# Kernel tuning notes

Hardware: AMD Instinct MI355X
Metric: run time of the kernel (lower is better)

The kernel has to match this reference:

```python
import jax, jax.numpy as jnp
import numpy as np
from functools import partial

L, D, H, F, K, T = 8, 512, 8, 2048, 11, 2048
DK = D // H
PAD = (K - 1) // 2  # 5, matches pad_zeros width
SCALE = DK ** -0.5  # q,k each prescaled by d_k^-0.25 in the torch code


def setup_inputs() -> dict:
    key = jax.random.key(0)
    ks = jax.random.split(key, 16)
    s = 0.02
    return {
        "x": jax.random.normal(ks[0], (1, T, D), jnp.float32),
        "ln1_g": jnp.ones((L, D), jnp.float32),
        "ln1_b": jnp.zeros((L, D), jnp.float32),
        "Wqkv": jax.random.normal(ks[1], (L, D, 3 * D), jnp.float32) * s,
        "bqkv": jnp.zeros((L, 3 * D), jnp.float32),
        "fsmn_w": jax.random.normal(ks[2], (L, D, K), jnp.float32) * s,
        "Wout": jax.random.normal(ks[3], (L, D, D), jnp.float32) * s,
        "bout": jnp.zeros((L, D), jnp.float32),
        "ln2_g": jnp.ones((L, D), jnp.float32),
        "ln2_b": jnp.zeros((L, D), jnp.float32),
        "W1": jax.random.normal(ks[4], (L, D, F), jnp.float32) * s,
        "b1": jnp.zeros((L, F), jnp.float32),
        "W2": jax.random.normal(ks[5], (L, F, D), jnp.float32) * s,
        "b2": jnp.zeros((L, D), jnp.float32),
        "after_g": jnp.ones((D,), jnp.float32),
        "after_b": jnp.zeros((D,), jnp.float32),
    }


def layernorm(x, g, b, eps=1e-5):
    m = jnp.mean(x, axis=-1, keepdims=True)
    v = jnp.var(x, axis=-1, keepdims=True)
    return (x - m) * jax.lax.rsqrt(v + eps) * g + b


def fsmn(v, w):
    # v: [1, T, D]; depthwise conv1d, kernel K, zero-pad PAD each side (matches pad_zeros cat)
    vc = jnp.transpose(v, (0, 2, 1))  # [1, D, T]
    out = jax.lax.conv_general_dilated(
        vc, w[:, None, :], window_strides=(1,), padding=[(PAD, PAD)],
        feature_group_count=D, dimension_numbers=("NCH", "OIH", "NCH"))
    return jnp.transpose(out, (0, 2, 1)) + v  # fsmn_block(...) + v


def encoder_layer(x, p):
    (g1, b1_, Wqkv, bqkv, fw, Wout, bout, g2, b2_, W1, c1, W2, c2) = p
    x1 = layernorm(x, g1, b1_)
    qkv = jnp.einsum("btd,de->bte", x1, Wqkv) + bqkv  # [1, T, 3D]
    q, k, v = jnp.split(qkv, 3, axis=-1)
    qh = q.reshape(T, H, DK).transpose(1, 0, 2)  # [H, T, dk]
    kh = k.reshape(T, H, DK).transpose(1, 0, 2)
    vh = v.reshape(T, H, DK).transpose(1, 0, 2)
    scores = jnp.einsum("htd,hsd->hts", qh, kh) * SCALE  # [H, T, T]
    attn = jnp.einsum("hts,hsd->htd", jax.nn.softmax(scores, axis=-1), vh)
    attn = attn.transpose(1, 0, 2).reshape(1, T, D)
    attn = jnp.einsum("btd,de->bte", attn, Wout) + bout
    mem = fsmn(v, fw)
    x = x + attn + mem
    h = layernorm(x, g2, b2_)
    h = jax.nn.relu(jnp.einsum("btd,df->btf", h, W1) + c1)
    x = x + jnp.einsum("btf,fd->btd", h, W2) + c2
    return x, None


def reference(x, ln1_g, ln1_b, Wqkv, bqkv, fsmn_w, Wout, bout, ln2_g, ln2_b, W1, b1, W2, b2, after_g, after_b):
    params = (ln1_g, ln1_b, Wqkv, bqkv, fsmn_w, Wout, bout, ln2_g, ln2_b, W1, b1, W2, b2)
    x, _ = jax.lax.scan(encoder_layer, x, params)
    return layernorm(x, after_g, after_b)
```

## Files before the change

kernel.cpp:

```cpp
#include <hip/hip_runtime.h>

using u16 = unsigned short;
using u32 = unsigned int;

typedef __bf16 bf16x8 __attribute__((ext_vector_type(8)));
typedef float f32x4 __attribute__((ext_vector_type(4)));

typedef __attribute__((address_space(3))) u32 as3_u32;
typedef __attribute__((address_space(1))) const u32 as1_u32;

__device__ __forceinline__ u16 f2bf(float f) {
  u32 u = __builtin_bit_cast(u32, f);
  u = u + 0x7FFFu + ((u >> 16) & 1u);
  return (u16)(u >> 16);
}
__device__ __forceinline__ float bf2f(u16 h) {
  return __builtin_bit_cast(float, (u32)h << 16);
}

__device__ __forceinline__ void gload16(const u16* g, u16* l) {
  __builtin_amdgcn_global_load_lds((as1_u32*)g, (as3_u32*)l, 16, 0, 0);
}

__global__ __launch_bounds__(256) void transpose_f32_bf16(
    const float* __restrict__ in, u16* __restrict__ out, int R, int C) {
  __shared__ u16 tile[32][33];
  long zofs = (long)blockIdx.z * R * C;
  int c0 = blockIdx.x * 32, r0 = blockIdx.y * 32;
  for (int i = threadIdx.y; i < 32; i += 8)
    tile[i][threadIdx.x] = f2bf(in[zofs + (long)(r0 + i) * C + c0 + threadIdx.x]);
  __syncthreads();
  for (int i = threadIdx.y; i < 32; i += 8)
    out[zofs + (long)(c0 + i) * R + r0 + threadIdx.x] = tile[threadIdx.x][i];
}

template <int MI, int NI, int VT>
__global__ __launch_bounds__(256) void gemm_bt(
    const u16* __restrict__ A, int lda,
    const u16* __restrict__ B, int ldb,
    const float* __restrict__ bias,
    u16* __restrict__ outBf, int ldob,
    float* __restrict__ outF, int ldof, int accF,
    u16* __restrict__ vtOut,
    int M, int N, int K, int kChunks, float scale, int relu) {
  __shared__ u16 As[MI * 32 * 64];
  __shared__ u16 Bs[NI * 32 * 64];
  __shared__ u16 Ts[VT ? NI * 32 : 1][72];
  const int m0 = blockIdx.y * (MI * 32), n0 = blockIdx.x * (NI * 32);
  const int tid = threadIdx.x, lane = tid & 63, wid = tid >> 6;
  const int wr = (wid >> 1) * (MI * 16), wc = (wid & 1) * (NI * 16);
  const int r16 = lane & 15, kg = lane >> 4;

  const int lrow = lane >> 3;
  const int lchunk = (lane & 7) ^ lrow;

  f32x4 acc[MI][NI];
#pragma unroll
  for (int i = 0; i < MI; ++i)
#pragma unroll
    for (int j = 0; j < NI; ++j) acc[i][j] = f32x4{0.f, 0.f, 0.f, 0.f};

  const int kcs = K / kChunks;
  const int kbase = kcs * blockIdx.z;
  const int nkt = kcs / 64;
  for (int kt = 0; kt < nkt; ++kt) {
    const int k0 = kbase + kt * 64;
    __syncthreads();
#pragma unroll
    for (int i = 0; i < MI; ++i) {
      const int r = i * 32 + wid * 8 + lrow;
      gload16(A + (long)(m0 + r) * lda + k0 + lchunk * 8, &As[wid * 512 + i * 2048]);
    }
#pragma unroll
    for (int j = 0; j < NI; ++j) {
      const int r = j * 32 + wid * 8 + lrow;
      gload16(B + (long)(n0 + r) * ldb + k0 + lchunk * 8, &Bs[wid * 512 + j * 2048]);
    }
    __syncthreads();

#pragma unroll
    for (int s = 0; s < 2; ++s) {
      bf16x8 af[MI], bfv[NI];
#pragma unroll
      for (int i = 0; i < MI; ++i) {
        const int r = wr + i * 16 + r16;
        af[i] = *reinterpret_cast<const bf16x8*>(
            &As[r * 64 + (((s * 4 + kg) ^ (r & 7)) << 3)]);
      }
#pragma unroll
      for (int j = 0; j < NI; ++j) {
        const int r = wc + j * 16 + r16;
        bfv[j] = *reinterpret_cast<const bf16x8*>(
            &Bs[r * 64 + (((s * 4 + kg) ^ (r & 7)) << 3)]);
      }
      __builtin_amdgcn_s_setprio(1);
#pragma unroll
      for (int i = 0; i < MI; ++i)
#pragma unroll
        for (int j = 0; j < NI; ++j)
          acc[i][j] = __builtin_amdgcn_mfma_f32_16x16x32_bf16(af[i], bfv[j], acc[i][j], 0, 0, 0);
      __builtin_amdgcn_s_setprio(0);
    }
  }

  const int rg = (lane >> 4) * 4;
  const bool doVT = VT && (n0 >= 1024);
#pragma unroll
  for (int i = 0; i < MI; ++i) {
#pragma unroll
    for (int j = 0; j < NI; ++j) {
      int col = n0 + wc + j * 16 + r16;
      float bv = (bias && blockIdx.z == 0) ? bias[col] : 0.f;
#pragma unroll
      for (int r = 0; r < 4; ++r) {
        int row = m0 + wr + i * 16 + rg + r;
        float v = acc[i][j][r] * scale + bv;
        if (outF) {
          long idx = (long)row * ldof + col;
          if (accF) atomicAdd(&outF[idx], v);
          else outF[idx] = v;
        }
        if (outBf) {
          if (relu && v < 0.f) v = 0.f;
          u16 hv = f2bf(v);
          outBf[(long)row * ldob + col] = hv;
          if (doVT) Ts[wc + j * 16 + r16][wr + i * 16 + rg + r] = hv;
        }
      }
    }
  }

  if constexpr (VT) {
    if (doVT) {
      __syncthreads();
      const int d0 = n0 - 1024;
      constexpr int CH = MI * 4;
      constexpr int TOT = NI * 32 * CH;
#pragma unroll
      for (int c = 0; c < TOT / 256; ++c) {
        int idx = tid * (TOT / 256) + c;
        int drow = idx / CH, off = (idx % CH) * 8;
        *reinterpret_cast<uint4*>(vtOut + (long)(d0 + drow) * 2048 + m0 + off) =
            *reinterpret_cast<const uint4*>(&Ts[drow][off]);
      }
    }
  }
}

constexpr int AFP = 72;

__global__ __launch_bounds__(256, 4) void flash_attn_split(
    const u16* __restrict__ qkv, const u16* __restrict__ vT,
    float* __restrict__ oPart, float* __restrict__ lPart) {
  __shared__ u16 Ks[2][64 * AFP];
  __shared__ u16 Vs[64 * AFP];
  __shared__ u16 Ps[4][16 * AFP];
  const int h = blockIdx.y;
  const int q0 = blockIdx.x * 64;
  const int split = blockIdx.z;
  const int tid = threadIdx.x;
  const int lane = tid & 63, wid = tid >> 6;
  const int r16 = lane & 15, kg8 = (lane >> 4) * 8;

  bf16x8 qa0, qa1;
  {
    union U { uint4 v; u16 hh[8]; } a, b;
    const u16* qrow = qkv + (long)(q0 + wid * 16 + r16) * 1536 + 64 * h;
    a.v = *reinterpret_cast<const uint4*>(qrow + kg8);
    b.v = *reinterpret_cast<const uint4*>(qrow + 32 + kg8);
#pragma unroll
    for (int i = 0; i < 8; ++i) {
      a.hh[i] = f2bf(bf2f(a.hh[i]) * 0.125f);
      b.hh[i] = f2bf(bf2f(b.hh[i]) * 0.125f);
    }
    qa0 = __builtin_bit_cast(bf16x8, a.v);
    qa1 = __builtin_bit_cast(bf16x8, b.v);
  }

  const int srow = tid >> 2;
  const int scol = (tid & 3) * 16;
  const u16* kgl = qkv + 512 + 64 * h + scol;
  const u16* vgl = vT + (long)(64 * h + srow) * 2048 + scol;

  uint4 kr0, kr1, vr0, vr1;
  auto LOAD = [&](int g) {
    const u16* kp = kgl + (long)(g * 64 + srow) * 1536;
    kr0 = *reinterpret_cast<const uint4*>(kp);
    kr1 = *reinterpret_cast<const uint4*>(kp + 8);
    const u16* vp = vgl + g * 64;
    vr0 = *reinterpret_cast<const uint4*>(vp);
    vr1 = *reinterpret_cast<const uint4*>(vp + 8);
  };
  auto STOREK = [&](int b) {
    *reinterpret_cast<uint4*>(&Ks[b][srow * AFP + scol]) = kr0;
    *reinterpret_cast<uint4*>(&Ks[b][srow * AFP + scol + 8]) = kr1;
  };
  auto STOREV = [&]() {
    *reinterpret_cast<uint4*>(&Vs[srow * AFP + scol]) = vr0;
    *reinterpret_cast<uint4*>(&Vs[srow * AFP + scol + 8]) = vr1;
  };

  f32x4 oacc[4];
#pragma unroll
  for (int j = 0; j < 4; ++j) oacc[j] = f32x4{0.f, 0.f, 0.f, 0.f};
  float lsum[4] = {0.f, 0.f, 0.f, 0.f};

  const int g0 = split * 8;
  LOAD(g0);
  STOREK(0);
  STOREV();
  __syncthreads();

  for (int t = 0; t < 8; ++t) {
    const int cur = t & 1;
    if (t < 7) LOAD(g0 + t + 1);

    f32x4 sacc[4];
#pragma unroll
    for (int j = 0; j < 4; ++j) sacc[j] = f32x4{0.f, 0.f, 0.f, 0.f};
    __builtin_amdgcn_s_setprio(1);
#pragma unroll
    for (int j = 0; j < 4; ++j) {
      bf16x8 b0 = *reinterpret_cast<const bf16x8*>(&Ks[cur][(j * 16 + r16) * AFP + kg8]);
      bf16x8 b1 = *reinterpret_cast<const bf16x8*>(&Ks[cur][(j * 16 + r16) * AFP + 32 + kg8]);
      sacc[j] = __builtin_amdgcn_mfma_f32_16x16x32_bf16(qa0, b0, sacc[j], 0, 0, 0);
      sacc[j] = __builtin_amdgcn_mfma_f32_16x16x32_bf16(qa1, b1, sacc[j], 0, 0, 0);
    }
    __builtin_amdgcn_s_setprio(0);

#pragma unroll
    for (int r = 0; r < 4; ++r) {
      float e0 = __expf(sacc[0][r]);
      float e1 = __expf(sacc[1][r]);
      float e2 = __expf(sacc[2][r]);
      float e3 = __expf(sacc[3][r]);
      lsum[r] += (e0 + e1) + (e2 + e3);
      int prow = (lane >> 4) * 4 + r;
      Ps[wid][prow * AFP + r16] = f2bf(e0);
      Ps[wid][prow * AFP + 16 + r16] = f2bf(e1);
      Ps[wid][prow * AFP + 32 + r16] = f2bf(e2);
      Ps[wid][prow * AFP + 48 + r16] = f2bf(e3);
    }

#pragma unroll
    for (int st = 0; st < 2; ++st) {
      bf16x8 pa = *reinterpret_cast<const bf16x8*>(&Ps[wid][r16 * AFP + st * 32 + kg8]);
      __builtin_amdgcn_s_setprio(1);
#pragma unroll
      for (int j = 0; j < 4; ++j) {
        bf16x8 bv = *reinterpret_cast<const bf16x8*>(&Vs[(j * 16 + r16) * AFP + st * 32 + kg8]);
        oacc[j] = __builtin_amdgcn_mfma_f32_16x16x32_bf16(pa, bv, oacc[j], 0, 0, 0);
      }
      __builtin_amdgcn_s_setprio(0);
    }

    if (t < 7) {
      STOREK(cur ^ 1);
      __syncthreads();
      STOREV();
      __syncthreads();
    }
  }

  const int rg = (lane >> 4) * 4;
#pragma unroll
  for (int r = 0; r < 4; ++r) {
    float ls = lsum[r];
#pragma unroll
    for (int o = 1; o < 16; o <<= 1) ls += __shfl_xor(ls, o);
    int row = q0 + wid * 16 + rg + r;
    if (r16 == 0) lPart[(long)(split * 8 + h) * 2048 + row] = ls;
#pragma unroll
    for (int j = 0; j < 4; ++j)
      oPart[(long)split * 2048 * 512 + (long)row * 512 + 64 * h + j * 16 + r16] =
          oacc[j][r];
  }
}

__global__ __launch_bounds__(256) void attn_norm_fsmn(
    const float* __restrict__ oPart, const float* __restrict__ lPart,
    u16* __restrict__ attn, float* __restrict__ x,
    const u16* __restrict__ qkv, const float* __restrict__ fw) {
  const int t = blockIdx.x;
  const int d = threadIdx.x * 2;
  const int h = d >> 6;
  float l = 0.f;
#pragma unroll
  for (int s = 0; s < 4; ++s) l += lPart[(long)(s * 8 + h) * 2048 + t];
  float ox = 0.f, oy = 0.f;
#pragma unroll
  for (int s = 0; s < 4; ++s) {
    const float2 v = *reinterpret_cast<const float2*>(
        oPart + (long)s * 2048 * 512 + (long)t * 512 + d);
    ox += v.x;
    oy += v.y;
  }
  const float inv = 1.f / l;
  u16* out = attn + (long)t * 512 + d;
  out[0] = f2bf(ox * inv);
  out[1] = f2bf(oy * inv);

  const u16* v = qkv + 1024 + d;
  float s0 = bf2f(v[(long)t * 1536]);
  float s1 = bf2f(v[(long)t * 1536 + 1]);
#pragma unroll
  for (int j = 0; j < 11; ++j) {
    int ts = t + j - 5;
    if (ts >= 0 && ts < 2048) {
      float w0 = fw[d * 11 + j], w1 = fw[(d + 1) * 11 + j];
      s0 += w0 * bf2f(v[(long)ts * 1536]);
      s1 += w1 * bf2f(v[(long)ts * 1536 + 1]);
    }
  }
  x[(long)t * 512 + d] += s0;
  x[(long)t * 512 + d + 1] += s1;
}

__device__ __forceinline__ void block_reduce2(float& s, float& ss) {
#pragma unroll
  for (int o = 32; o; o >>= 1) {
    s += __shfl_xor(s, o);
    ss += __shfl_xor(ss, o);
  }
  __shared__ float sm[8];
  int wid = threadIdx.x >> 6;
  if ((threadIdx.x & 63) == 0) {
    sm[wid] = s;
    sm[wid + 4] = ss;
  }
  __syncthreads();
  s = sm[0] + sm[1] + sm[2] + sm[3];
  ss = sm[4] + sm[5] + sm[6] + sm[7];
}

template <int OUTBF>
__global__ __launch_bounds__(256) void layernorm_k(
    const float* __restrict__ xin, const float* __restrict__ g,
    const float* __restrict__ bta, void* __restrict__ out) {
  const int row = blockIdx.x, tid = threadIdx.x;
  const float2 v = *reinterpret_cast<const float2*>(xin + (long)row * 512 + tid * 2);
  float s = v.x + v.y, ss = v.x * v.x + v.y * v.y;
  block_reduce2(s, ss);
  const float mean = s * (1.f / 512.f);
  const float var = ss * (1.f / 512.f) - mean * mean;
  const float inv = rsqrtf(var + 1e-5f);
  const float2 gg = *reinterpret_cast<const float2*>(g + tid * 2);
  const float2 bb = *reinterpret_cast<const float2*>(bta + tid * 2);
  const float y0 = (v.x - mean) * inv * gg.x + bb.x;
  const float y1 = (v.y - mean) * inv * gg.y + bb.y;
  if (OUTBF) {
    u16* o = (u16*)out + (long)row * 512 + tid * 2;
    o[0] = f2bf(y0);
    o[1] = f2bf(y1);
  } else {
    *reinterpret_cast<float2*>((float*)out + (long)row * 512 + tid * 2) =
        make_float2(y0, y1);
  }
}


extern "C" void kernel_launch(void* const* d_in, const int* in_sizes, int n_in,
                              void* d_out, int out_size, void* d_ws, size_t ws_size,
                              hipStream_t stream) {
  const float* in_x = (const float*)d_in[0];
  const float* ln1_g = (const float*)d_in[1];
  const float* ln1_b = (const float*)d_in[2];
  const float* Wqkv = (const float*)d_in[3];
  const float* bqkv = (const float*)d_in[4];
  const float* fsmn_w = (const float*)d_in[5];
  const float* Wout = (const float*)d_in[6];
  const float* bout = (const float*)d_in[7];
  const float* ln2_g = (const float*)d_in[8];
  const float* ln2_b = (const float*)d_in[9];
  const float* W1 = (const float*)d_in[10];
  const float* b1 = (const float*)d_in[11];
  const float* W2 = (const float*)d_in[12];
  const float* b2 = (const float*)d_in[13];
  const float* after_g = (const float*)d_in[14];
  const float* after_b = (const float*)d_in[15];

  const int T = 2048, D = 512, F = 2048, L = 8;

  char* p = (char*)d_ws;
  auto alloc = [&](size_t bytes) {
    char* r = p;
    p += (bytes + 255) & ~size_t(255);
    return r;
  };
  u16* WqkvT = (u16*)alloc(8L * 1536 * 512 * 2);
  u16* WoutT = (u16*)alloc(8L * 512 * 512 * 2);
  u16* W1T = (u16*)alloc(8L * 2048 * 512 * 2);
  u16* W2T = (u16*)alloc(8L * 512 * 2048 * 2);
  float* x = (float*)alloc((long)T * D * 4);
  u16* x1 = (u16*)alloc((long)T * D * 2);
  u16* qkv = (u16*)alloc((long)T * 1536 * 2);
  u16* vT = (u16*)alloc((long)D * T * 2);
  u16* attn = (u16*)alloc((long)T * D * 2);
  u16* hb = (u16*)alloc((long)T * F * 2);
  float* oPart = (float*)alloc(4L * T * D * 4);
  float* lPart = (float*)alloc(4L * 8 * T * 4);

  hipMemcpyAsync(x, in_x, (long)T * D * 4, hipMemcpyDeviceToDevice, stream);
  dim3 tb(32, 8);
  transpose_f32_bf16<<<dim3(1536 / 32, 512 / 32, 8), tb, 0, stream>>>(Wqkv, WqkvT, 512, 1536);
  transpose_f32_bf16<<<dim3(512 / 32, 512 / 32, 8), tb, 0, stream>>>(Wout, WoutT, 512, 512);
  transpose_f32_bf16<<<dim3(2048 / 32, 512 / 32, 8), tb, 0, stream>>>(W1, W1T, 512, 2048);
  transpose_f32_bf16<<<dim3(512 / 32, 2048 / 32, 8), tb, 0, stream>>>(W2, W2T, 2048, 512);

  for (int l = 0; l < L; ++l) {
    layernorm_k<1><<<T, 256, 0, stream>>>(x, ln1_g + 512 * l, ln1_b + 512 * l, x1);
    gemm_bt<2, 2, 1><<<dim3(24, 32, 1), 256, 0, stream>>>(
        x1, 512, WqkvT + (long)l * 1536 * 512, 512, bqkv + 1536 * l,
        qkv, 1536, (float*)nullptr, 0, 0, vT, T, 1536, 512, 1, 1.f, 0);
    flash_attn_split<<<dim3(32, 8, 4), 256, 0, stream>>>(qkv, vT, oPart, lPart);
    attn_norm_fsmn<<<T, 256, 0, stream>>>(oPart, lPart, attn, x, qkv,
                                          fsmn_w + (long)l * 512 * 11);
    gemm_bt<2, 2, 0><<<dim3(8, 32, 4), 256, 0, stream>>>(
        attn, 512, WoutT + (long)l * 512 * 512, 512, bout + 512 * l,
        (u16*)nullptr, 0, x, 512, 1, (u16*)nullptr, T, 512, 512, 4, 1.f, 0);
    layernorm_k<1><<<T, 256, 0, stream>>>(x, ln2_g + 512 * l, ln2_b + 512 * l, x1);
    gemm_bt<2, 2, 0><<<dim3(32, 32, 1), 256, 0, stream>>>(
        x1, 512, W1T + (long)l * 2048 * 512, 512, b1 + 2048 * l,
        hb, 2048, (float*)nullptr, 0, 0, (u16*)nullptr, T, 2048, 512, 1, 1.f, 1);
    gemm_bt<2, 2, 0><<<dim3(8, 32, 4), 256, 0, stream>>>(
        hb, 2048, W2T + (long)l * 512 * 2048, 2048, b2 + 512 * l,
        (u16*)nullptr, 0, x, 512, 1, (u16*)nullptr, T, 512, 2048, 4, 1.f, 0);
  }
  layernorm_k<0><<<T, 256, 0, stream>>>(x, after_g, after_b, (float*)d_out);
}
```

Before: 869.6 us.

## Double-buffer GEMM LDS tiles and store attention partials in bf16

The GEMM kernel now keeps two LDS buffers and issues the global-to-LDS loads for the next K tile before computing the current one, with one barrier per iteration. This overlaps memory latency with MFMA work. Separately, the split flash-attention partial outputs are written as bf16 instead of fp32, which halves the traffic between the attention and normalization kernels. The costs are doubled LDS use in the GEMM, which may lower occupancy, and reduced precision in the partial sums.

```diff
diff --git a/kernel.cpp b/kernel.cpp
--- a/kernel.cpp
+++ b/kernel.cpp
@@ -43,8 +43,8 @@
     float* __restrict__ outF, int ldof, int accF,
     u16* __restrict__ vtOut,
     int M, int N, int K, int kChunks, float scale, int relu) {
-  __shared__ u16 As[MI * 32 * 64];
-  __shared__ u16 Bs[NI * 32 * 64];
+  __shared__ u16 As[2][MI * 32 * 64];
+  __shared__ u16 Bs[2][NI * 32 * 64];
   __shared__ u16 Ts[VT ? NI * 32 : 1][72];
   const int m0 = blockIdx.y * (MI * 32), n0 = blockIdx.x * (NI * 32);
   const int tid = threadIdx.x, lane = tid & 63, wid = tid >> 6;
@@ -63,20 +63,28 @@
   const int kcs = K / kChunks;
   const int kbase = kcs * blockIdx.z;
   const int nkt = kcs / 64;
-  for (int kt = 0; kt < nkt; ++kt) {
-    const int k0 = kbase + kt * 64;
-    __syncthreads();
+
+  auto STAGE = [&](int b, int k0) {
 #pragma unroll
     for (int i = 0; i < MI; ++i) {
       const int r = i * 32 + wid * 8 + lrow;
-      gload16(A + (long)(m0 + r) * lda + k0 + lchunk * 8, &As[wid * 512 + i * 2048]);
+      gload16(A + (long)(m0 + r) * lda + k0 + lchunk * 8,
+              &As[b][wid * 512 + i * 2048]);
     }
 #pragma unroll
     for (int j = 0; j < NI; ++j) {
       const int r = j * 32 + wid * 8 + lrow;
-      gload16(B + (long)(n0 + r) * ldb + k0 + lchunk * 8, &Bs[wid * 512 + j * 2048]);
-    }
-    __syncthreads();
+      gload16(B + (long)(n0 + r) * ldb + k0 + lchunk * 8,
+              &Bs[b][wid * 512 + j * 2048]);
+    }
+  };
+
+  STAGE(0, kbase);
+  __syncthreads();
+
+  for (int kt = 0; kt < nkt; ++kt) {
+    const int cur = kt & 1;
+    if (kt + 1 < nkt) STAGE(cur ^ 1, kbase + (kt + 1) * 64);
 
 #pragma unroll
     for (int s = 0; s < 2; ++s) {
@@ -85,13 +93,13 @@
       for (int i = 0; i < MI; ++i) {
         const int r = wr + i * 16 + r16;
         af[i] = *reinterpret_cast<const bf16x8*>(
-            &As[r * 64 + (((s * 4 + kg) ^ (r & 7)) << 3)]);
+            &As[cur][r * 64 + (((s * 4 + kg) ^ (r & 7)) << 3)]);
       }
 #pragma unroll
       for (int j = 0; j < NI; ++j) {
         const int r = wc + j * 16 + r16;
         bfv[j] = *reinterpret_cast<const bf16x8*>(
-            &Bs[r * 64 + (((s * 4 + kg) ^ (r & 7)) << 3)]);
+            &Bs[cur][r * 64 + (((s * 4 + kg) ^ (r & 7)) << 3)]);
       }
       __builtin_amdgcn_s_setprio(1);
 #pragma unroll
@@ -101,6 +109,7 @@
           acc[i][j] = __builtin_amdgcn_mfma_f32_16x16x32_bf16(af[i], bfv[j], acc[i][j], 0, 0, 0);
       __builtin_amdgcn_s_setprio(0);
     }
+    __syncthreads();
   }
 
   const int rg = (lane >> 4) * 4;
@@ -151,7 +160,7 @@
 
 __global__ __launch_bounds__(256, 4) void flash_attn_split(
     const u16* __restrict__ qkv, const u16* __restrict__ vT,
-    float* __restrict__ oPart, float* __restrict__ lPart) {
+    u16* __restrict__ oPart, float* __restrict__ lPart) {
   __shared__ u16 Ks[2][64 * AFP];
   __shared__ u16 Vs[64 * AFP];
   __shared__ u16 Ps[4][16 * AFP];
@@ -273,12 +282,12 @@
 #pragma unroll
     for (int j = 0; j < 4; ++j)
       oPart[(long)split * 2048 * 512 + (long)row * 512 + 64 * h + j * 16 + r16] =
-          oacc[j][r];
+          f2bf(oacc[j][r]);
   }
 }
 
 __global__ __launch_bounds__(256) void attn_norm_fsmn(
-    const float* __restrict__ oPart, const float* __restrict__ lPart,
+    const u16* __restrict__ oPart, const float* __restrict__ lPart,
     u16* __restrict__ attn, float* __restrict__ x,
     const u16* __restrict__ qkv, const float* __restrict__ fw) {
   const int t = blockIdx.x;
@@ -290,10 +299,10 @@
   float ox = 0.f, oy = 0.f;
 #pragma unroll
   for (int s = 0; s < 4; ++s) {
-    const float2 v = *reinterpret_cast<const float2*>(
+    const u32 v = *reinterpret_cast<const u32*>(
         oPart + (long)s * 2048 * 512 + (long)t * 512 + d);
-    ox += v.x;
-    oy += v.y;
+    ox += bf2f((u16)v);
+    oy += bf2f((u16)(v >> 16));
   }
   const float inv = 1.f / l;
   u16* out = attn + (long)t * 512 + d;
@@ -397,7 +406,7 @@
   u16* vT = (u16*)alloc((long)D * T * 2);
   u16* attn = (u16*)alloc((long)T * D * 2);
   u16* hb = (u16*)alloc((long)T * F * 2);
-  float* oPart = (float*)alloc(4L * T * D * 4);
+  u16* oPart = (u16*)alloc(4L * T * D * 2);
   float* lPart = (float*)alloc(4L * 8 * T * 4);
 
   hipMemcpyAsync(x, in_x, (long)T * D * 4, hipMemcpyDeviceToDevice, stream);
```

After: 852.4 us. 1.02x faster.
